# Kernel optimization log

Hardware: AMD Instinct MI355X
Metric: run time of the kernel (lower is better)

Reference implementation:

```python
import jax, jax.numpy as jnp
import numpy as np

B, LMAX, NCOND, NHID = 256, 512, 300, 600

def setup_inputs() -> dict:
    key = jax.random.key(0)
    ks = jax.random.split(key, 7)
    x = jax.random.normal(ks[0], (B, NCOND), dtype=jnp.float32)
    context = jax.random.normal(ks[1], (B, LMAX, NCOND), dtype=jnp.float32)
    lengths = jax.random.randint(ks[2], (B,), 0, LMAX, dtype=jnp.int32)
    W1 = jax.random.normal(ks[3], (NCOND, NHID), dtype=jnp.float32) * (1.0 / np.sqrt(NCOND))
    b1 = jax.random.normal(ks[4], (NHID,), dtype=jnp.float32) * 0.02
    Wa = jax.random.normal(ks[5], (NHID, NCOND), dtype=jnp.float32) * (1.0 / np.sqrt(NHID))
    ba = jax.random.normal(ks[6], (NCOND,), dtype=jnp.float32) * 0.02
    return {"x": x, "context": context, "lengths": lengths, "W1": W1, "b1": b1, "Wa": Wa, "ba": ba}

def reference(x, context, lengths, W1, b1, Wa, ba):
    # lengths clamped to >=1 (a ragged context is always non-empty)
    lens = jnp.maximum(lengths, 1)
    # valid-position mask over padded context: [B, L, 1]
    valid = (jnp.arange(LMAX)[None, :] < lens[:, None])[..., None].astype(context.dtype)
    # per-token MLP: relu(ctx @ W1 + b1)  -> [B, L, nhid]
    h = jax.nn.relu(jnp.einsum('blc,ch->blh', context, W1) + b1)
    # masked mean over valid tokens (ragged mean-pool) -> [B, nhid]
    pooled = jnp.sum(h * valid, axis=1) / lens[:, None].astype(context.dtype)
    # sigmoid gate -> [B, ncond], applied to x embeddings
    gate = jax.nn.sigmoid(jnp.einsum('bh,hc->bc', pooled, Wa) + ba)
    return gate * x
```

## Files before the change

### kernel.cpp

```cpp
#include <hip/hip_runtime.h>
#include <math.h>

#define BB     256
#define LMAX   512
#define NCOND  300
#define NHID   600
#define KPAD   320
#define KLDS   328
#define NCOLP  640
#define NTILE  40
#define NKC    10
#define CHUNK  64

typedef short s16x8 __attribute__((ext_vector_type(8)));
typedef float f32x4 __attribute__((ext_vector_type(4)));

__device__ inline unsigned short f2bf(float f) {
    unsigned int x = __float_as_uint(f);
    x += 0x7fffu + ((x >> 16) & 1u);
    return (unsigned short)(x >> 16);
}

__global__ __launch_bounds__(256) void k0_prep(const float* __restrict__ W1,
                                               const int* __restrict__ lengths,
                                               unsigned short* __restrict__ w1t,
                                               int* __restrict__ sched)
{
    if (blockIdx.x < 100) {
        const int t     = blockIdx.x * 256 + threadIdx.x;
        const int lane  = t & 63;
        const int g     = t >> 6;
        const int ntile = g / NKC;
        const int kc    = g - ntile * NKC;
        const int n     = ntile * 16 + (lane & 15);
        const int kbase = kc * 32 + (lane >> 4) * 8;
        union { unsigned short us[8]; s16x8 v8; } u;
#pragma unroll
        for (int j = 0; j < 8; ++j) {
            const int k = kbase + j;
            const float w = (n < NHID && k < NCOND) ? W1[(size_t)k * NHID + n] : 0.f;
            u.us[j] = f2bf(w);
        }
        *(s16x8*)(w1t + (size_t)t * 8) = u.v8;
    } else {
        const int i = threadIdx.x;
        int li = lengths[i]; if (li < 1) li = 1;
        int rank = 0;
        for (int j = 0; j < BB; ++j) {
            int lj = lengths[j]; if (lj < 1) lj = 1;
            rank += (lj > li) || (lj == li && j < i);
        }
        sched[rank] = i;
    }
}

__global__ __launch_bounds__(256) void k1_mfma_pool(
    const float* __restrict__ ctx, const int* __restrict__ lengths,
    const unsigned short* __restrict__ w1t, const float* __restrict__ b1,
    const int* __restrict__ sched, float* __restrict__ pooled)
{
    const int b    = sched[blockIdx.x >> 1];
    const int ch   = blockIdx.x & 1;
    const int tid  = threadIdx.x;
    const int lane = tid & 63;
    const int wv   = tid >> 6;
    const int ln15 = lane & 15;
    const int kg   = lane >> 4;

    int count = lengths[b]; if (count < 1) count = 1;
    const int nchunks = (count + CHUNK - 1) / CHUNK;

    __shared__ __align__(16) unsigned short atile[CHUNK * KLDS];

    const int ntile0 = ch * 20 + wv * 5;
    const unsigned short* bbase = w1t + ((size_t)ntile0 * NKC * 64 + lane) * 8;
    const unsigned short* arow  = atile + ln15 * KLDS + kg * 8;

    float b1c[5];
#pragma unroll
    for (int nt = 0; nt < 5; ++nt) {
        const int colg = ch * 320 + wv * 80 + nt * 16 + ln15;
        b1c[nt] = (colg < NHID) ? b1[colg] : 0.f;
    }

    float psum[5] = {0.f, 0.f, 0.f, 0.f, 0.f};

    for (int c = 0; c < nchunks; ++c) {
        const int l0    = c * CHUNK;
        const int valid = min(count - l0, CHUNK);

#pragma unroll
        for (int p = 0; p < 10; ++p) {
            const int i  = p * 256 + tid;
            const int r  = i / 40;
            const int c8 = i - r * 40;
            union { unsigned short us[8]; s16x8 v8; } u;
            if (r < valid && c8 < 38) {
                const float* src = ctx + ((size_t)b * LMAX + l0 + r) * NCOND + c8 * 8;
                const float4 v0 = *(const float4*)src;
                float4 v1 = make_float4(0.f, 0.f, 0.f, 0.f);
                if (c8 < 37) v1 = *(const float4*)(src + 4);
                u.us[0] = f2bf(v0.x); u.us[1] = f2bf(v0.y);
                u.us[2] = f2bf(v0.z); u.us[3] = f2bf(v0.w);
                u.us[4] = f2bf(v1.x); u.us[5] = f2bf(v1.y);
                u.us[6] = f2bf(v1.z); u.us[7] = f2bf(v1.w);
            } else {
#pragma unroll
                for (int j = 0; j < 8; ++j) u.us[j] = 0;
            }
            *(s16x8*)(atile + r * KLDS + c8 * 8) = u.v8;
        }
        __syncthreads();

        f32x4 acc[5][4];
#pragma unroll
        for (int nt = 0; nt < 5; ++nt)
#pragma unroll
            for (int mt = 0; mt < 4; ++mt) acc[nt][mt] = (f32x4){0.f, 0.f, 0.f, 0.f};

        s16x8 bf[2][5], af[2][4];
#pragma unroll
        for (int nt = 0; nt < 5; ++nt) bf[0][nt] = *(const s16x8*)(bbase + nt * 5120);
#pragma unroll
        for (int mt = 0; mt < 4; ++mt) af[0][mt] = *(const s16x8*)(arow + mt * 16 * KLDS);

#pragma unroll
        for (int kc = 0; kc < NKC; ++kc) {
            const int cur = kc & 1, nxt = cur ^ 1;
            if (kc < NKC - 1) {
#pragma unroll
                for (int nt = 0; nt < 5; ++nt)
                    bf[nxt][nt] = *(const s16x8*)(bbase + nt * 5120 + (kc + 1) * 512);
#pragma unroll
                for (int mt = 0; mt < 4; ++mt)
                    af[nxt][mt] = *(const s16x8*)(arow + mt * 16 * KLDS + (kc + 1) * 32);
            }
#pragma unroll
            for (int nt = 0; nt < 5; ++nt)
#pragma unroll
                for (int mt = 0; mt < 4; ++mt)
                    acc[nt][mt] = __builtin_amdgcn_mfma_f32_16x16x32_bf16(
                        af[cur][mt], bf[cur][nt], acc[nt][mt], 0, 0, 0);
        }

#pragma unroll
        for (int nt = 0; nt < 5; ++nt) {
            float s = 0.f;
#pragma unroll
            for (int mt = 0; mt < 4; ++mt) {
                const int rbase = mt * 16 + kg * 4;
#pragma unroll
                for (int r = 0; r < 4; ++r) {
                    const float h = fmaxf(acc[nt][mt][r] + b1c[nt], 0.f);
                    if (rbase + r < valid) s += h;
                }
            }
            psum[nt] += s;
        }
        __syncthreads();
    }

    const float inv = 1.0f / (float)count;
#pragma unroll
    for (int nt = 0; nt < 5; ++nt) {
        float s = psum[nt];
        s += __shfl_xor(s, 16, 64);
        s += __shfl_xor(s, 32, 64);
        if (kg == 0) {
            const int colg = ch * 320 + wv * 80 + nt * 16 + ln15;
            if (colg < NHID)
                pooled[(size_t)b * NHID + colg] = s * inv;
        }
    }
}

__global__ __launch_bounds__(320) void k2_gate(
    const float* __restrict__ x, const float* __restrict__ pooled,
    const float* __restrict__ Wa, const float* __restrict__ ba,
    float* __restrict__ out)
{
    const int b   = blockIdx.x;
    const int tid = threadIdx.x;

    __shared__ float pl[NHID];
    for (int h = tid; h < NHID; h += 320)
        pl[h] = pooled[(size_t)b * NHID + h];
    __syncthreads();

    if (tid < NCOND) {
        const int n = tid;
        float a0 = ba[n], a1 = 0.f;
        const float4* p4 = (const float4*)pl;
        for (int h4 = 0; h4 < NHID / 4; h4 += 2) {
            const float4 pv0 = p4[h4];
            const float4 pv1 = p4[h4 + 1];
            const int hb = h4 * 4;
            a0 = fmaf(pv0.x, Wa[(size_t)(hb + 0) * NCOND + n], a0);
            a0 = fmaf(pv0.y, Wa[(size_t)(hb + 1) * NCOND + n], a0);
            a0 = fmaf(pv0.z, Wa[(size_t)(hb + 2) * NCOND + n], a0);
            a0 = fmaf(pv0.w, Wa[(size_t)(hb + 3) * NCOND + n], a0);
            a1 = fmaf(pv1.x, Wa[(size_t)(hb + 4) * NCOND + n], a1);
            a1 = fmaf(pv1.y, Wa[(size_t)(hb + 5) * NCOND + n], a1);
            a1 = fmaf(pv1.z, Wa[(size_t)(hb + 6) * NCOND + n], a1);
            a1 = fmaf(pv1.w, Wa[(size_t)(hb + 7) * NCOND + n], a1);
        }
        const float acc  = a0 + a1;
        const float gate = 1.0f / (1.0f + expf(-acc));
        out[(size_t)b * NCOND + n] = gate * x[(size_t)b * NCOND + n];
    }
}

extern "C" void kernel_launch(void* const* d_in, const int* in_sizes, int n_in,
                              void* d_out, int out_size, void* d_ws, size_t ws_size,
                              hipStream_t stream)
{
    const float* x       = (const float*)d_in[0];
    const float* ctx     = (const float*)d_in[1];
    const int*   lengths = (const int*)  d_in[2];
    const float* W1      = (const float*)d_in[3];
    const float* b1      = (const float*)d_in[4];
    const float* Wa      = (const float*)d_in[5];
    const float* ba      = (const float*)d_in[6];
    float*       out     = (float*)d_out;

    unsigned short* w1t    = (unsigned short*)d_ws;
    int*            sched  = (int*)((char*)d_ws + 409600);
    float*          pooled = (float*)((char*)d_ws + 409600 + 1024);

    k0_prep<<<101, 256, 0, stream>>>(W1, lengths, w1t, sched);
    k1_mfma_pool<<<512, 256, 0, stream>>>(ctx, lengths, w1t, b1, sched, pooled);
    k2_gate<<<BB, 320, 0, stream>>>(x, pooled, Wa, ba, out);
}
```

Before: 320.2 us.

## Split per-batch pooling across sequence chunks with partial sums reduced in gate kernel

The pooling kernel now launches one block per (batch, 64-token chunk, column half) and exits early for chunks beyond the length, in place of one block looping over all chunks of a length-sorted batch. Per-chunk partial sums go to a workspace buffer, and the gate kernel, which now handles two batches per block with more accumulators, reduces them and divides by the length. This removes the sorting schedule and the serial chunk loop to expose more parallelism and balance ragged lengths, at the cost of partial-sum traffic, many empty blocks, and an extra reduction in the gate kernel.

Measured after the change: 298.8 us. 6.7% less time.

```diff
diff --git a/kernel.cpp b/kernel.cpp
--- a/kernel.cpp
+++ b/kernel.cpp
@@ -5,12 +5,12 @@
 #define LMAX   512
 #define NCOND  300
 #define NHID   600
+#define NSEG   8
+#define CHUNK  64
 #define KPAD   320
 #define KLDS   328
 #define NCOLP  640
-#define NTILE  40
 #define NKC    10
-#define CHUNK  64
 
 typedef short s16x8 __attribute__((ext_vector_type(8)));
 typedef float f32x4 __attribute__((ext_vector_type(4)));
@@ -21,190 +21,191 @@
     return (unsigned short)(x >> 16);
 }
 
-__global__ __launch_bounds__(256) void k0_prep(const float* __restrict__ W1,
-                                               const int* __restrict__ lengths,
-                                               unsigned short* __restrict__ w1t,
-                                               int* __restrict__ sched)
-{
-    if (blockIdx.x < 100) {
-        const int t     = blockIdx.x * 256 + threadIdx.x;
-        const int lane  = t & 63;
-        const int g     = t >> 6;
-        const int ntile = g / NKC;
-        const int kc    = g - ntile * NKC;
-        const int n     = ntile * 16 + (lane & 15);
-        const int kbase = kc * 32 + (lane >> 4) * 8;
-        union { unsigned short us[8]; s16x8 v8; } u;
-#pragma unroll
-        for (int j = 0; j < 8; ++j) {
-            const int k = kbase + j;
-            const float w = (n < NHID && k < NCOND) ? W1[(size_t)k * NHID + n] : 0.f;
-            u.us[j] = f2bf(w);
-        }
-        *(s16x8*)(w1t + (size_t)t * 8) = u.v8;
-    } else {
-        const int i = threadIdx.x;
-        int li = lengths[i]; if (li < 1) li = 1;
-        int rank = 0;
-        for (int j = 0; j < BB; ++j) {
-            int lj = lengths[j]; if (lj < 1) lj = 1;
-            rank += (lj > li) || (lj == li && j < i);
-        }
-        sched[rank] = i;
-    }
-}
-
-__global__ __launch_bounds__(256) void k1_mfma_pool(
+__global__ __launch_bounds__(256) void k0_w1t(const float* __restrict__ W1,
+                                              unsigned short* __restrict__ w1t)
+{
+    const int t     = blockIdx.x * 256 + threadIdx.x;
+    const int lane  = t & 63;
+    const int g     = t >> 6;
+    const int ntile = g / NKC;
+    const int kc    = g - ntile * NKC;
+    const int n     = ntile * 16 + (lane & 15);
+    const int kbase = kc * 32 + (lane >> 4) * 8;
+    union { unsigned short us[8]; s16x8 v8; } u;
+#pragma unroll
+    for (int j = 0; j < 8; ++j) {
+        const int k = kbase + j;
+        const float w = (n < NHID && k < NCOND) ? W1[(size_t)k * NHID + n] : 0.f;
+        u.us[j] = f2bf(w);
+    }
+    *(s16x8*)(w1t + (size_t)t * 8) = u.v8;
+}
+
+__global__ __launch_bounds__(256, 3) void k1_mfma_pool(
     const float* __restrict__ ctx, const int* __restrict__ lengths,
     const unsigned short* __restrict__ w1t, const float* __restrict__ b1,
-    const int* __restrict__ sched, float* __restrict__ pooled)
-{
-    const int b    = sched[blockIdx.x >> 1];
-    const int ch   = blockIdx.x & 1;
+    float* __restrict__ partial)
+{
+    const int b  = blockIdx.x;
+    const int s  = blockIdx.y;
+    const int ch = blockIdx.z;
+
+    int count = lengths[b]; if (count < 1) count = 1;
+    const int l0 = s * CHUNK;
+    if (l0 >= count) return;
+    const int valid = min(count - l0, CHUNK);
+
     const int tid  = threadIdx.x;
     const int lane = tid & 63;
     const int wv   = tid >> 6;
     const int ln15 = lane & 15;
     const int kg   = lane >> 4;
 
-    int count = lengths[b]; if (count < 1) count = 1;
-    const int nchunks = (count + CHUNK - 1) / CHUNK;
-
     __shared__ __align__(16) unsigned short atile[CHUNK * KLDS];
+
+#pragma unroll
+    for (int p = 0; p < 10; ++p) {
+        const int i  = p * 256 + tid;
+        const int r  = i / 40;
+        const int c8 = i - r * 40;
+        union { unsigned short us[8]; s16x8 v8; } u;
+        if (r < valid && c8 < 38) {
+            const float* src = ctx + ((size_t)b * LMAX + l0 + r) * NCOND + c8 * 8;
+            const float4 v0 = *(const float4*)src;
+            float4 v1 = make_float4(0.f, 0.f, 0.f, 0.f);
+            if (c8 < 37) v1 = *(const float4*)(src + 4);
+            u.us[0] = f2bf(v0.x); u.us[1] = f2bf(v0.y);
+            u.us[2] = f2bf(v0.z); u.us[3] = f2bf(v0.w);
+            u.us[4] = f2bf(v1.x); u.us[5] = f2bf(v1.y);
+            u.us[6] = f2bf(v1.z); u.us[7] = f2bf(v1.w);
+        } else {
+#pragma unroll
+            for (int j = 0; j < 8; ++j) u.us[j] = 0;
+        }
+        *(s16x8*)(atile + r * KLDS + c8 * 8) = u.v8;
+    }
+    __syncthreads();
 
     const int ntile0 = ch * 20 + wv * 5;
     const unsigned short* bbase = w1t + ((size_t)ntile0 * NKC * 64 + lane) * 8;
     const unsigned short* arow  = atile + ln15 * KLDS + kg * 8;
 
-    float b1c[5];
+    f32x4 acc[5][4];
+#pragma unroll
+    for (int nt = 0; nt < 5; ++nt)
+#pragma unroll
+        for (int mt = 0; mt < 4; ++mt) acc[nt][mt] = (f32x4){0.f, 0.f, 0.f, 0.f};
+
+    s16x8 bf[2][5];
+#pragma unroll
+    for (int nt = 0; nt < 5; ++nt) bf[0][nt] = *(const s16x8*)(bbase + nt * 5120);
+
+#pragma unroll
+    for (int kc = 0; kc < NKC; ++kc) {
+        const int cur = kc & 1, nxt = cur ^ 1;
+        if (kc < NKC - 1) {
+#pragma unroll
+            for (int nt = 0; nt < 5; ++nt)
+                bf[nxt][nt] = *(const s16x8*)(bbase + nt * 5120 + (kc + 1) * 512);
+        }
+        s16x8 af[4];
+#pragma unroll
+        for (int mt = 0; mt < 4; ++mt)
+            af[mt] = *(const s16x8*)(arow + mt * 16 * KLDS + kc * 32);
+#pragma unroll
+        for (int nt = 0; nt < 5; ++nt)
+#pragma unroll
+            for (int mt = 0; mt < 4; ++mt)
+                acc[nt][mt] = __builtin_amdgcn_mfma_f32_16x16x32_bf16(
+                    af[mt], bf[cur][nt], acc[nt][mt], 0, 0, 0);
+    }
+
 #pragma unroll
     for (int nt = 0; nt < 5; ++nt) {
         const int colg = ch * 320 + wv * 80 + nt * 16 + ln15;
-        b1c[nt] = (colg < NHID) ? b1[colg] : 0.f;
-    }
-
-    float psum[5] = {0.f, 0.f, 0.f, 0.f, 0.f};
-
-    for (int c = 0; c < nchunks; ++c) {
-        const int l0    = c * CHUNK;
-        const int valid = min(count - l0, CHUNK);
-
-#pragma unroll
-        for (int p = 0; p < 10; ++p) {
-            const int i  = p * 256 + tid;
-            const int r  = i / 40;
-            const int c8 = i - r * 40;
-            union { unsigned short us[8]; s16x8 v8; } u;
-            if (r < valid && c8 < 38) {
-                const float* src = ctx + ((size_t)b * LMAX + l0 + r) * NCOND + c8 * 8;
-                const float4 v0 = *(const float4*)src;
-                float4 v1 = make_float4(0.f, 0.f, 0.f, 0.f);
-                if (c8 < 37) v1 = *(const float4*)(src + 4);
-                u.us[0] = f2bf(v0.x); u.us[1] = f2bf(v0.y);
-                u.us[2] = f2bf(v0.z); u.us[3] = f2bf(v0.w);
-                u.us[4] = f2bf(v1.x); u.us[5] = f2bf(v1.y);
-                u.us[6] = f2bf(v1.z); u.us[7] = f2bf(v1.w);
-            } else {
-#pragma unroll
-                for (int j = 0; j < 8; ++j) u.us[j] = 0;
+        const float b1c = (colg < NHID) ? b1[colg] : 0.f;
+        float ssum = 0.f;
+#pragma unroll
+        for (int mt = 0; mt < 4; ++mt) {
+            const int rbase = mt * 16 + kg * 4;
+#pragma unroll
+            for (int r = 0; r < 4; ++r) {
+                const float h = fmaxf(acc[nt][mt][r] + b1c, 0.f);
+                if (rbase + r < valid) ssum += h;
             }
-            *(s16x8*)(atile + r * KLDS + c8 * 8) = u.v8;
-        }
-        __syncthreads();
-
-        f32x4 acc[5][4];
-#pragma unroll
-        for (int nt = 0; nt < 5; ++nt)
-#pragma unroll
-            for (int mt = 0; mt < 4; ++mt) acc[nt][mt] = (f32x4){0.f, 0.f, 0.f, 0.f};
-
-        s16x8 bf[2][5], af[2][4];
-#pragma unroll
-        for (int nt = 0; nt < 5; ++nt) bf[0][nt] = *(const s16x8*)(bbase + nt * 5120);
-#pragma unroll
-        for (int mt = 0; mt < 4; ++mt) af[0][mt] = *(const s16x8*)(arow + mt * 16 * KLDS);
-
-#pragma unroll
-        for (int kc = 0; kc < NKC; ++kc) {
-            const int cur = kc & 1, nxt = cur ^ 1;
-            if (kc < NKC - 1) {
-#pragma unroll
-                for (int nt = 0; nt < 5; ++nt)
-                    bf[nxt][nt] = *(const s16x8*)(bbase + nt * 5120 + (kc + 1) * 512);
-#pragma unroll
-                for (int mt = 0; mt < 4; ++mt)
-                    af[nxt][mt] = *(const s16x8*)(arow + mt * 16 * KLDS + (kc + 1) * 32);
-            }
-#pragma unroll
-            for (int nt = 0; nt < 5; ++nt)
-#pragma unroll
-                for (int mt = 0; mt < 4; ++mt)
-                    acc[nt][mt] = __builtin_amdgcn_mfma_f32_16x16x32_bf16(
-                        af[cur][mt], bf[cur][nt], acc[nt][mt], 0, 0, 0);
-        }
-
-#pragma unroll
-        for (int nt = 0; nt < 5; ++nt) {
-            float s = 0.f;
-#pragma unroll
-            for (int mt = 0; mt < 4; ++mt) {
-                const int rbase = mt * 16 + kg * 4;
-#pragma unroll
-                for (int r = 0; r < 4; ++r) {
-                    const float h = fmaxf(acc[nt][mt][r] + b1c[nt], 0.f);
-                    if (rbase + r < valid) s += h;
-                }
-            }
-            psum[nt] += s;
-        }
-        __syncthreads();
-    }
-
-    const float inv = 1.0f / (float)count;
-#pragma unroll
-    for (int nt = 0; nt < 5; ++nt) {
-        float s = psum[nt];
-        s += __shfl_xor(s, 16, 64);
-        s += __shfl_xor(s, 32, 64);
-        if (kg == 0) {
-            const int colg = ch * 320 + wv * 80 + nt * 16 + ln15;
-            if (colg < NHID)
-                pooled[(size_t)b * NHID + colg] = s * inv;
-        }
-    }
-}
-
-__global__ __launch_bounds__(320) void k2_gate(
-    const float* __restrict__ x, const float* __restrict__ pooled,
-    const float* __restrict__ Wa, const float* __restrict__ ba,
-    float* __restrict__ out)
-{
-    const int b   = blockIdx.x;
+        }
+        ssum += __shfl_xor(ssum, 16, 64);
+        ssum += __shfl_xor(ssum, 32, 64);
+        if (kg == 0 && colg < NHID)
+            partial[((size_t)s * BB + b) * NHID + colg] = ssum;
+    }
+}
+
+__global__ __launch_bounds__(640) void k2_gate(
+    const float* __restrict__ x, const int* __restrict__ lengths,
+    const float* __restrict__ partial, const float* __restrict__ Wa,
+    const float* __restrict__ ba, float* __restrict__ out)
+{
+    const int b0  = blockIdx.x * 2;
     const int tid = threadIdx.x;
 
-    __shared__ float pl[NHID];
-    for (int h = tid; h < NHID; h += 320)
-        pl[h] = pooled[(size_t)b * NHID + h];
+    __shared__ float pl[2][NHID];
+
+    if (tid < NHID) {
+#pragma unroll
+        for (int bb = 0; bb < 2; ++bb) {
+            int count = lengths[b0 + bb]; if (count < 1) count = 1;
+            const int nch = (count + CHUNK - 1) >> 6;
+            float ssum = 0.f;
+            for (int sp = 0; sp < nch; ++sp)
+                ssum += partial[((size_t)sp * BB + (b0 + bb)) * NHID + tid];
+            pl[bb][tid] = ssum / (float)count;
+        }
+    }
     __syncthreads();
 
-    if (tid < NCOND) {
-        const int n = tid;
-        float a0 = ba[n], a1 = 0.f;
-        const float4* p4 = (const float4*)pl;
-        for (int h4 = 0; h4 < NHID / 4; h4 += 2) {
+    if (tid < 2 * NCOND) {
+        const int bb = tid / NCOND;
+        const int n  = tid - bb * NCOND;
+        const int b  = b0 + bb;
+        float a0 = ba[n], a1 = 0.f, a2 = 0.f, a3 = 0.f;
+        const float4* p4 = (const float4*)pl[bb];
+        for (int h4 = 0; h4 < 148; h4 += 4) {
             const float4 pv0 = p4[h4];
             const float4 pv1 = p4[h4 + 1];
+            const float4 pv2 = p4[h4 + 2];
+            const float4 pv3 = p4[h4 + 3];
             const int hb = h4 * 4;
-            a0 = fmaf(pv0.x, Wa[(size_t)(hb + 0) * NCOND + n], a0);
-            a0 = fmaf(pv0.y, Wa[(size_t)(hb + 1) * NCOND + n], a0);
-            a0 = fmaf(pv0.z, Wa[(size_t)(hb + 2) * NCOND + n], a0);
-            a0 = fmaf(pv0.w, Wa[(size_t)(hb + 3) * NCOND + n], a0);
-            a1 = fmaf(pv1.x, Wa[(size_t)(hb + 4) * NCOND + n], a1);
-            a1 = fmaf(pv1.y, Wa[(size_t)(hb + 5) * NCOND + n], a1);
-            a1 = fmaf(pv1.z, Wa[(size_t)(hb + 6) * NCOND + n], a1);
-            a1 = fmaf(pv1.w, Wa[(size_t)(hb + 7) * NCOND + n], a1);
-        }
-        const float acc  = a0 + a1;
+            a0 = fmaf(pv0.x, Wa[(size_t)(hb +  0) * NCOND + n], a0);
+            a0 = fmaf(pv0.y, Wa[(size_t)(hb +  1) * NCOND + n], a0);
+            a0 = fmaf(pv0.z, Wa[(size_t)(hb +  2) * NCOND + n], a0);
+            a0 = fmaf(pv0.w, Wa[(size_t)(hb +  3) * NCOND + n], a0);
+            a1 = fmaf(pv1.x, Wa[(size_t)(hb +  4) * NCOND + n], a1);
+            a1 = fmaf(pv1.y, Wa[(size_t)(hb +  5) * NCOND + n], a1);
+            a1 = fmaf(pv1.z, Wa[(size_t)(hb +  6) * NCOND + n], a1);
+            a1 = fmaf(pv1.w, Wa[(size_t)(hb +  7) * NCOND + n], a1);
+            a2 = fmaf(pv2.x, Wa[(size_t)(hb +  8) * NCOND + n], a2);
+            a2 = fmaf(pv2.y, Wa[(size_t)(hb +  9) * NCOND + n], a2);
+            a2 = fmaf(pv2.z, Wa[(size_t)(hb + 10) * NCOND + n], a2);
+            a2 = fmaf(pv2.w, Wa[(size_t)(hb + 11) * NCOND + n], a2);
+            a3 = fmaf(pv3.x, Wa[(size_t)(hb + 12) * NCOND + n], a3);
+            a3 = fmaf(pv3.y, Wa[(size_t)(hb + 13) * NCOND + n], a3);
+            a3 = fmaf(pv3.z, Wa[(size_t)(hb + 14) * NCOND + n], a3);
+            a3 = fmaf(pv3.w, Wa[(size_t)(hb + 15) * NCOND + n], a3);
+        }
+        {
+            const float4 pv0 = p4[148];
+            const float4 pv1 = p4[149];
+            a0 = fmaf(pv0.x, Wa[(size_t)592 * NCOND + n], a0);
+            a0 = fmaf(pv0.y, Wa[(size_t)593 * NCOND + n], a0);
+            a0 = fmaf(pv0.z, Wa[(size_t)594 * NCOND + n], a0);
+            a0 = fmaf(pv0.w, Wa[(size_t)595 * NCOND + n], a0);
+            a1 = fmaf(pv1.x, Wa[(size_t)596 * NCOND + n], a1);
+            a1 = fmaf(pv1.y, Wa[(size_t)597 * NCOND + n], a1);
+            a1 = fmaf(pv1.z, Wa[(size_t)598 * NCOND + n], a1);
+            a1 = fmaf(pv1.w, Wa[(size_t)599 * NCOND + n], a1);
+        }
+        const float acc  = (a0 + a1) + (a2 + a3);
         const float gate = 1.0f / (1.0f + expf(-acc));
         out[(size_t)b * NCOND + n] = gate * x[(size_t)b * NCOND + n];
     }
@@ -223,11 +224,10 @@
     const float* ba      = (const float*)d_in[6];
     float*       out     = (float*)d_out;
 
-    unsigned short* w1t    = (unsigned short*)d_ws;
-    int*            sched  = (int*)((char*)d_ws + 409600);
-    float*          pooled = (float*)((char*)d_ws + 409600 + 1024);
-
-    k0_prep<<<101, 256, 0, stream>>>(W1, lengths, w1t, sched);
-    k1_mfma_pool<<<512, 256, 0, stream>>>(ctx, lengths, w1t, b1, sched, pooled);
-    k2_gate<<<BB, 320, 0, stream>>>(x, pooled, Wa, ba, out);
-}
+    unsigned short* w1t     = (unsigned short*)d_ws;
+    float*          partial = (float*)((char*)d_ws + 409600);
+
+    k0_w1t<<<100, 256, 0, stream>>>(W1, w1t);
+    k1_mfma_pool<<<dim3(BB, NSEG, 2), 256, 0, stream>>>(ctx, lengths, w1t, b1, partial);
+    k2_gate<<<BB / 2, 640, 0, stream>>>(x, lengths, partial, Wa, ba, out);
+}
```
